# Optimization experiments

Measured on AMD Instinct MI355X. Metric: run time of the kernel, lower is better.

## Reference

```python
import jax, jax.numpy as jnp
import numpy as np

D_MODEL = 1024
N_HEADS = 16
HEAD_DIM = D_MODEL // N_HEADS
SCALE = HEAD_DIM ** -0.5


def setup_inputs() -> dict:
    key = jax.random.key(0)
    ks = jax.random.split(key, 5)
    B, T = 2, 2048
    w_std = D_MODEL ** -0.5  # ~ torch Linear init scale
    return {
        "x": jax.random.normal(ks[0], (B, T, D_MODEL), dtype=jnp.float32),
        "W_q": jax.random.normal(ks[1], (D_MODEL, D_MODEL), dtype=jnp.float32) * w_std,
        "W_k": jax.random.normal(ks[2], (D_MODEL, D_MODEL), dtype=jnp.float32) * w_std,
        "W_v": jax.random.normal(ks[3], (D_MODEL, D_MODEL), dtype=jnp.float32) * w_std,
        "W_o": jax.random.normal(ks[4], (D_MODEL, D_MODEL), dtype=jnp.float32) * w_std,
    }


def reference(x, W_q, W_k, W_v, W_o):
    # torch Linear: y = x @ W.T  (weight stored as (out, in))
    B, T, _ = x.shape

    def split_heads(y):  # (B,T,D) -> (B,H,T,hd)
        return y.reshape(B, T, N_HEADS, HEAD_DIM).transpose(0, 2, 1, 3)

    q = split_heads(x @ W_q.T)
    k = split_heads(x @ W_k.T)
    v = split_heads(x @ W_v.T)

    attn = jnp.einsum("bhqd,bhkd->bhqk", q, k) * SCALE  # (B,H,T,T)
    attn = jax.nn.softmax(attn, axis=-1)
    out = jnp.einsum("bhqk,bhkd->bhqd", attn, v)  # (B,H,T,hd)
    out = out.transpose(0, 2, 1, 3).reshape(B, T, D_MODEL)
    return out @ W_o.T
```

## Files before the change

kernel.cpp:

```cpp
#include <hip/hip_runtime.h>
#include <hip/hip_bf16.h>

#define D_MODEL 1024
#define N_HEADS 16
#define HEAD_DIM 64
#define SEQ 2048
#define BATCH 2

typedef __attribute__((ext_vector_type(8))) short bf16x8;
typedef __attribute__((ext_vector_type(4))) short bf16x4;
typedef __attribute__((ext_vector_type(4))) float f32x4;
typedef __attribute__((ext_vector_type(16))) float f32x16;

typedef __attribute__((address_space(3))) unsigned lds_uint;
typedef __attribute__((address_space(1))) const unsigned global_cuint;

__device__ __forceinline__ void async_cp16(const ushort* g, ushort* l) {
  __builtin_amdgcn_global_load_lds((global_cuint*)g, (lds_uint*)l, 16, 0, 0);
}

__device__ __forceinline__ ushort f2b(float f) {
  union { float f; unsigned u; } x; x.f = f;
  unsigned r = x.u + 0x7fffu + ((x.u >> 16) & 1u);
  return (ushort)(r >> 16);
}

__device__ __forceinline__ unsigned pk2(float a, float b) {
  __hip_bfloat162 h = __float22bfloat162_rn(float2{a, b});
  union { __hip_bfloat162 h; unsigned u; } x; x.h = h;
  return x.u;
}

__device__ __forceinline__ float blo(unsigned u) {
  union { unsigned u; float f; } x; x.u = u << 16; return x.f;
}
__device__ __forceinline__ float bhi(unsigned u) {
  union { unsigned u; float f; } x; x.u = u & 0xffff0000u; return x.f;
}

__device__ __forceinline__ int sigma23(int t) {
  return (t & ~12) | ((t & 4) << 1) | ((t & 8) >> 1);
}

__device__ __forceinline__ int swz64(int row, int colbyte) {
  return row * 64 + ((colbyte ^ ((row & 7) << 4)) >> 1);
}

__global__ __launch_bounds__(256) void cast_all(const float* __restrict__ x,
                                                const float* __restrict__ Wq,
                                                const float* __restrict__ Wk,
                                                const float* __restrict__ Wv,
                                                const float* __restrict__ Wo,
                                                ushort* __restrict__ xb,
                                                ushort* __restrict__ wqkv,
                                                ushort* __restrict__ wob) {
  int idx = blockIdx.x * 256 + threadIdx.x;
  const float* in;
  uint2* out;
  if (idx < (1 << 20)) {
    in = x; out = (uint2*)xb;
  } else {
    int j = idx - (1 << 20);
    int w = j >> 18;
    idx = j & 0x3FFFF;
    switch (w) {
      case 0: in = Wq; out = (uint2*)wqkv; break;
      case 1: in = Wk; out = (uint2*)(wqkv) + (1 << 18); break;
      case 2: in = Wv; out = (uint2*)(wqkv) + (2 << 18); break;
      default: in = Wo; out = (uint2*)wob; break;
    }
  }
  float4 v = ((const float4*)in)[idx];
  uint2 o; o.x = pk2(v.x, v.y); o.y = pk2(v.z, v.w);
  out[idx] = o;
}

__global__ __launch_bounds__(512, 2) void gemm_qkv(const ushort* __restrict__ A,
                                                   const ushort* __restrict__ Bw,
                                                   ushort* __restrict__ Qh,
                                                   ushort* __restrict__ Kh,
                                                   ushort* __restrict__ Vth,
                                                   float qscale) {
  constexpr int K = 1024;
  const int bm = blockIdx.y * 128;
  const int bn = blockIdx.x * 128;
  const int tid = threadIdx.x;
  const int wave = tid >> 6;
  const int lane = tid & 63;
  const int l16 = lane & 15;
  const int quad = lane >> 4;

  __shared__ ushort As[2][128 * 64];
  __shared__ ushort Bs[2][128 * 64];

  const int wm = (wave & 1) * 64;
  const int wn = (wave >> 1) * 32;

  f32x4 acc[4][2];
#pragma unroll
  for (int r = 0; r < 4; ++r)
#pragma unroll
    for (int c = 0; c < 2; ++c) acc[r][c] = (f32x4){0.f, 0.f, 0.f, 0.f};

  const int srow = wave * 8 + (lane >> 3);
  const int csw = (((lane & 7) ^ (lane >> 3)) << 3);

#pragma unroll
  for (int j = 0; j < 2; ++j) {
    async_cp16(A  + (size_t)(bm + j * 64 + srow) * K + csw, &As[0][(j * 64 + wave * 8) * 64]);
    async_cp16(Bw + (size_t)(bn + j * 64 + srow) * K + csw, &Bs[0][(j * 64 + wave * 8) * 64]);
  }

  constexpr int NIT = K / 64;
  for (int kt = 0; kt < NIT; ++kt) {
    __syncthreads();
    const int buf = kt & 1;
    if (kt + 1 < NIT) {
      const int k0 = (kt + 1) * 64;
#pragma unroll
      for (int j = 0; j < 2; ++j) {
        async_cp16(A  + (size_t)(bm + j * 64 + srow) * K + k0 + csw, &As[buf ^ 1][(j * 64 + wave * 8) * 64]);
        async_cp16(Bw + (size_t)(bn + j * 64 + srow) * K + k0 + csw, &Bs[buf ^ 1][(j * 64 + wave * 8) * 64]);
      }
    }

    bf16x8 a[2][4], b[2][2];
#pragma unroll
    for (int ks = 0; ks < 2; ++ks) {
#pragma unroll
      for (int r = 0; r < 4; ++r)
        a[ks][r] = *(const bf16x8*)(&As[buf][swz64(wm + r * 16 + l16, ks * 64 + quad * 16)]);
#pragma unroll
      for (int c = 0; c < 2; ++c)
        b[ks][c] = *(const bf16x8*)(&Bs[buf][swz64(wn + c * 16 + l16, ks * 64 + quad * 16)]);
    }
#pragma unroll
    for (int ks = 0; ks < 2; ++ks)
#pragma unroll
      for (int r = 0; r < 4; ++r)
#pragma unroll
        for (int c = 0; c < 2; ++c)
          acc[r][c] = __builtin_amdgcn_mfma_f32_16x16x32_bf16(a[ks][r], b[ks][c], acc[r][c], 0, 0, 0);
  }

#pragma unroll
  for (int r = 0; r < 4; ++r) {
#pragma unroll
    for (int c = 0; c < 2; ++c) {
      int ncol = bn + wn + c * 16 + l16;
      int w = ncol >> 10;
      int f = ncol & 1023;
      int h = f >> 6, d = f & 63;
      if (w == 2) {
        int m0 = bm + wm + r * 16 + quad * 4;
        int b = m0 >> 11, t0 = m0 & 2047;
        uint2 pp;
        pp.x = pk2(acc[r][c][0], acc[r][c][1]);
        pp.y = pk2(acc[r][c][2], acc[r][c][3]);
        *(uint2*)(&Vth[((size_t)(b * 1024 + f) << 11) + t0]) = pp;
      } else {
#pragma unroll
        for (int rr = 0; rr < 4; ++rr) {
          float v = acc[r][c][rr];
          int m = bm + wm + r * 16 + quad * 4 + rr;
          int b = m >> 11, t = m & 2047;
          if (w == 0)
            Qh[((size_t)(b * 16 + h) * SEQ + t) * 64 + d] = f2b(v * qscale);
          else
            Kh[((size_t)(b * 16 + h) * SEQ + sigma23(t)) * 64 + d] = f2b(v);
        }
      }
    }
  }
}

__global__ __launch_bounds__(256) void gemm_out(const ushort* __restrict__ A,
                                                const ushort* __restrict__ Bw,
                                                float* __restrict__ out) {
  constexpr int K = 1024;
  const int bm = blockIdx.y * 64;
  const int bn = blockIdx.x * 128;
  const int tid = threadIdx.x;
  const int wave = tid >> 6;
  const int lane = tid & 63;
  const int l16 = lane & 15;
  const int quad = lane >> 4;

  __shared__ ushort As[2][64 * 64];
  __shared__ ushort Bs[2][128 * 64];

  const int wm = (wave & 1) * 32;
  const int wn = (wave >> 1) * 64;

  f32x4 acc[2][4];
#pragma unroll
  for (int r = 0; r < 2; ++r)
#pragma unroll
    for (int c = 0; c < 4; ++c) acc[r][c] = (f32x4){0.f, 0.f, 0.f, 0.f};

  const int srow = wave * 8 + (lane >> 3);
  const int csw = (((lane & 7) ^ (lane >> 3)) << 3);

#pragma unroll
  for (int j = 0; j < 2; ++j)
    async_cp16(A + (size_t)(bm + j * 32 + srow) * K + csw, &As[0][(j * 32 + wave * 8) * 64]);
#pragma unroll
  for (int j = 0; j < 4; ++j)
    async_cp16(Bw + (size_t)(bn + j * 32 + srow) * K + csw, &Bs[0][(j * 32 + wave * 8) * 64]);

  constexpr int NIT = K / 64;
  for (int kt = 0; kt < NIT; ++kt) {
    __syncthreads();
    const int buf = kt & 1;
    if (kt + 1 < NIT) {
      const int k0 = (kt + 1) * 64;
#pragma unroll
      for (int j = 0; j < 2; ++j)
        async_cp16(A + (size_t)(bm + j * 32 + srow) * K + k0 + csw, &As[buf ^ 1][(j * 32 + wave * 8) * 64]);
#pragma unroll
      for (int j = 0; j < 4; ++j)
        async_cp16(Bw + (size_t)(bn + j * 32 + srow) * K + k0 + csw, &Bs[buf ^ 1][(j * 32 + wave * 8) * 64]);
    }

    bf16x8 a[2][2], b[2][4];
#pragma unroll
    for (int ks = 0; ks < 2; ++ks) {
#pragma unroll
      for (int r = 0; r < 2; ++r)
        a[ks][r] = *(const bf16x8*)(&As[buf][swz64(wm + r * 16 + l16, ks * 64 + quad * 16)]);
#pragma unroll
      for (int c = 0; c < 4; ++c)
        b[ks][c] = *(const bf16x8*)(&Bs[buf][swz64(wn + c * 16 + l16, ks * 64 + quad * 16)]);
    }
#pragma unroll
    for (int ks = 0; ks < 2; ++ks)
#pragma unroll
      for (int r = 0; r < 2; ++r)
#pragma unroll
        for (int c = 0; c < 4; ++c)
          acc[r][c] = __builtin_amdgcn_mfma_f32_16x16x32_bf16(a[ks][r], b[ks][c], acc[r][c], 0, 0, 0);
  }

#pragma unroll
  for (int r = 0; r < 2; ++r)
#pragma unroll
    for (int c = 0; c < 4; ++c)
#pragma unroll
      for (int rr = 0; rr < 4; ++rr) {
        int m = bm + wm + r * 16 + quad * 4 + rr;
        int n = bn + wn + c * 16 + l16;
        out[(size_t)m * D_MODEL + n] = acc[r][c][rr];
      }
}

__global__ __launch_bounds__(256, 2) void attn_kernel(const ushort* __restrict__ Qh,
                                                      const ushort* __restrict__ Kh,
                                                      const ushort* __restrict__ Vth,
                                                      ushort* __restrict__ O1,
                                                      ushort* __restrict__ O2,
                                                      float* __restrict__ l1,
                                                      float* __restrict__ l2) {
  const int id = blockIdx.x;
  const int stream = id & 63;
  const int qb = id >> 6;
  const int bh = stream >> 1;
  const int half = stream & 1;
  const int q0 = qb * 128;
  ushort* __restrict__ Op = half ? O2 : O1;
  float* __restrict__ lp = half ? l2 : l1;

  const int tid = threadIdx.x;
  const int wave = tid >> 6;
  const int lane = tid & 63;
  const int l31 = lane & 31;
  const int hi = lane >> 5;

  __shared__ ushort KVbuf[2][2][64 * 64];

  bf16x8 qf[4];
#pragma unroll
  for (int dc = 0; dc < 4; ++dc)
    qf[dc] = *(const bf16x8*)(Qh + ((size_t)bh * SEQ + q0 + wave * 32 + l31) * 64 + dc * 16 + hi * 8);

  f32x16 o0 = {0.f, 0.f, 0.f, 0.f, 0.f, 0.f, 0.f, 0.f,
               0.f, 0.f, 0.f, 0.f, 0.f, 0.f, 0.f, 0.f};
  f32x16 o1 = o0;
  float lacc = 0.f;

  const int chunk = wave * 2;
  const int r8 = lane >> 3;
  const int csw = (((lane & 7) ^ r8) << 3);
  const ushort* kbase = Kh + ((size_t)bh * SEQ + half * 1024) * 64;
  const ushort* vbase = Vth + (size_t)bh * 64 * SEQ + half * 1024;
  const ushort* ksrc = kbase + (size_t)(chunk * 8 + r8) * 64 + csw;
  const ushort* vsrc = vbase + (size_t)(chunk * 8 + r8) * SEQ + csw;

  async_cp16(ksrc,           &KVbuf[0][0][chunk * 512]);
  async_cp16(ksrc + 8 * 64,  &KVbuf[0][0][(chunk + 1) * 512]);
  async_cp16(vsrc,           &KVbuf[0][1][chunk * 512]);
  async_cp16(vsrc + 8 * SEQ, &KVbuf[0][1][(chunk + 1) * 512]);

  constexpr int NIT = 1024 / 64;
  for (int kt = 0; kt < NIT; ++kt) {
    __syncthreads();
    const int buf = kt & 1;
    if (kt + 1 < NIT) {
      const ushort* ks = ksrc + (size_t)(kt + 1) * 64 * 64;
      const ushort* vs = vsrc + (kt + 1) * 64;
      async_cp16(ks,           &KVbuf[buf ^ 1][0][chunk * 512]);
      async_cp16(ks + 8 * 64,  &KVbuf[buf ^ 1][0][(chunk + 1) * 512]);
      async_cp16(vs,           &KVbuf[buf ^ 1][1][chunk * 512]);
      async_cp16(vs + 8 * SEQ, &KVbuf[buf ^ 1][1][(chunk + 1) * 512]);
    }
    const ushort* Kt = KVbuf[buf][0];
    const ushort* Vt = KVbuf[buf][1];

#pragma unroll
    for (int kt2 = 0; kt2 < 2; ++kt2) {
      bf16x8 ka0 = *(const bf16x8*)(&Kt[swz64(kt2 * 32 + l31, 0 * 32 + hi * 16)]);
      bf16x8 ka1 = *(const bf16x8*)(&Kt[swz64(kt2 * 32 + l31, 1 * 32 + hi * 16)]);
      bf16x8 ka2 = *(const bf16x8*)(&Kt[swz64(kt2 * 32 + l31, 2 * 32 + hi * 16)]);
      bf16x8 ka3 = *(const bf16x8*)(&Kt[swz64(kt2 * 32 + l31, 3 * 32 + hi * 16)]);
      f32x16 z = {0.f, 0.f, 0.f, 0.f, 0.f, 0.f, 0.f, 0.f,
                  0.f, 0.f, 0.f, 0.f, 0.f, 0.f, 0.f, 0.f};
      z = __builtin_amdgcn_mfma_f32_32x32x16_bf16(ka0, qf[0], z, 0, 0, 0);
      z = __builtin_amdgcn_mfma_f32_32x32x16_bf16(ka1, qf[1], z, 0, 0, 0);
      z = __builtin_amdgcn_mfma_f32_32x32x16_bf16(ka2, qf[2], z, 0, 0, 0);
      z = __builtin_amdgcn_mfma_f32_32x32x16_bf16(ka3, qf[3], z, 0, 0, 0);

      float e[16];
#pragma unroll
      for (int r = 0; r < 16; ++r) e[r] = __builtin_amdgcn_exp2f(z[r]);
      lacc += (((e[0] + e[1]) + (e[2] + e[3])) + ((e[4] + e[5]) + (e[6] + e[7])))
            + (((e[8] + e[9]) + (e[10] + e[11])) + ((e[12] + e[13]) + (e[14] + e[15])));

#pragma unroll
      for (int lw = 0; lw < 2; ++lw) {
        const int base = lw * 8;
        union { unsigned u[4]; bf16x8 v; } pu;
        pu.u[0] = pk2(e[base + 0], e[base + 1]);
        pu.u[1] = pk2(e[base + 2], e[base + 3]);
        pu.u[2] = pk2(e[base + 4], e[base + 5]);
        pu.u[3] = pk2(e[base + 6], e[base + 7]);
        const int wb = (kt2 * 2 + lw) * 32;
        bf16x8 vb0 = *(const bf16x8*)(&Vt[swz64(0 + l31, wb + hi * 16)]);
        bf16x8 vb1 = *(const bf16x8*)(&Vt[swz64(32 + l31, wb + hi * 16)]);
        o0 = __builtin_amdgcn_mfma_f32_32x32x16_bf16(pu.v, vb0, o0, 0, 0, 0);
        o1 = __builtin_amdgcn_mfma_f32_32x32x16_bf16(pu.v, vb1, o1, 0, 0, 0);
      }
    }
  }

  {
    float ltot = lacc + __shfl_xor(lacc, 32, 64);
    if (hi == 0)
      lp[(size_t)bh * SEQ + q0 + wave * 32 + l31] = ltot;
  }

  __syncthreads();
  ushort* Ob = &KVbuf[0][0][0];
#pragma unroll
  for (int r = 0; r < 16; ++r) {
    int row = wave * 32 + (r & 3) + 8 * (r >> 2) + 4 * hi;
    Ob[row * 64 + l31] = f2b(o0[r]);
    Ob[row * 64 + 32 + l31] = f2b(o1[r]);
  }
  __syncthreads();
  {
    uint4* dst = (uint4*)(Op + ((size_t)bh * SEQ + q0) * 64);
    const uint4* src = (const uint4*)Ob;
#pragma unroll
    for (int i = 0; i < 4; ++i)
      dst[i * 256 + tid] = src[i * 256 + tid];
  }
}

__global__ __launch_bounds__(256) void recombine(const ushort* __restrict__ O1,
                                                 const ushort* __restrict__ O2,
                                                 const float* __restrict__ l1,
                                                 const float* __restrict__ l2,
                                                 ushort* __restrict__ ctx) {
  int idx = blockIdx.x * 256 + threadIdx.x;
  int row = idx >> 3;
  int d8 = idx & 7;
  uint4 a = ((const uint4*)O1)[idx];
  uint4 b = ((const uint4*)O2)[idx];
  float linv = 1.f / (l1[row] + l2[row]);
  uint4 res;
  unsigned* ap = (unsigned*)&a;
  unsigned* bp = (unsigned*)&b;
  unsigned* rp = (unsigned*)&res;
#pragma unroll
  for (int i = 0; i < 4; ++i) {
    float lo = (blo(ap[i]) + blo(bp[i])) * linv;
    float hi = (bhi(ap[i]) + bhi(bp[i])) * linv;
    rp[i] = pk2(lo, hi);
  }
  int bh = row >> 11, t = row & 2047;
  int bb = bh >> 4, h = bh & 15;
  ((uint4*)ctx)[(size_t)(bb * SEQ + t) * 128 + h * 8 + d8] = res;
}

extern "C" void kernel_launch(void* const* d_in, const int* in_sizes, int n_in,
                              void* d_out, int out_size, void* d_ws, size_t ws_size,
                              hipStream_t stream) {
  const float* x  = (const float*)d_in[0];
  const float* Wq = (const float*)d_in[1];
  const float* Wk = (const float*)d_in[2];
  const float* Wv = (const float*)d_in[3];
  const float* Wo = (const float*)d_in[4];
  float* out = (float*)d_out;

  char* ws = (char*)d_ws;
  const size_t MB = 1 << 20;
  ushort* xb   = (ushort*)(ws);
  ushort* wqkv = (ushort*)(ws +  8 * MB);
  ushort* wob  = (ushort*)(ws + 14 * MB);
  ushort* Qh   = (ushort*)(ws + 16 * MB);
  ushort* Kh   = (ushort*)(ws + 24 * MB);
  ushort* Vth  = (ushort*)(ws + 32 * MB);
  ushort* ctx  = (ushort*)(ws + 40 * MB);

  ushort* O1 = (ushort*)d_out;
  ushort* O2 = xb;
  float*  l1 = (float*)wqkv;
  float*  l2 = (float*)(ws + 8 * MB + 256 * 1024);

  cast_all<<<8192, 256, 0, stream>>>(x, Wq, Wk, Wv, Wo, xb, wqkv, wob);

  const float qscale = 0.125f * 1.44269504089f;
  gemm_qkv<<<dim3(3072 / 128, 4096 / 128), 512, 0, stream>>>(xb, wqkv, Qh, Kh, Vth, qscale);

  attn_kernel<<<(SEQ / 128) * BATCH * N_HEADS * 2, 256, 0, stream>>>(
      Qh, Kh, Vth, O1, O2, l1, l2);

  recombine<<<(BATCH * N_HEADS * SEQ * 64 / 8) / 256, 256, 0, stream>>>(O1, O2, l1, l2, ctx);

  gemm_out<<<dim3(1024 / 128, 4096 / 64), 256, 0, stream>>>(ctx, wob, out);
}
```

Measured before the change: 185.6 us.

## Process two 32-row query groups per wave in attention, halving block threads

The attention kernel now runs 2 waves (128 threads) per block instead of 4, and each wave handles 64 query rows as two 32-row groups. The K and V fragments loaded from shared memory are reused across both groups, which cuts LDS reads per MFMA. Each thread now issues twice as many async copies for the K/V tile. The cost is higher register pressure from doubled Q fragments and accumulators, and fewer waves per block to hide latency.

```diff
diff --git a/kernel.cpp b/kernel.cpp
--- a/kernel.cpp
+++ b/kernel.cpp
@@ -253,7 +253,7 @@
       }
 }
 
-__global__ __launch_bounds__(256, 2) void attn_kernel(const ushort* __restrict__ Qh,
+__global__ __launch_bounds__(128, 2) void attn_kernel(const ushort* __restrict__ Qh,
                                                       const ushort* __restrict__ Kh,
                                                       const ushort* __restrict__ Vth,
                                                       ushort* __restrict__ O1,
@@ -277,28 +277,35 @@
 
   __shared__ ushort KVbuf[2][2][64 * 64];
 
-  bf16x8 qf[4];
-#pragma unroll
-  for (int dc = 0; dc < 4; ++dc)
-    qf[dc] = *(const bf16x8*)(Qh + ((size_t)bh * SEQ + q0 + wave * 32 + l31) * 64 + dc * 16 + hi * 8);
-
-  f32x16 o0 = {0.f, 0.f, 0.f, 0.f, 0.f, 0.f, 0.f, 0.f,
-               0.f, 0.f, 0.f, 0.f, 0.f, 0.f, 0.f, 0.f};
-  f32x16 o1 = o0;
-  float lacc = 0.f;
-
-  const int chunk = wave * 2;
+  bf16x8 qf[2][4];
+#pragma unroll
+  for (int g = 0; g < 2; ++g)
+#pragma unroll
+    for (int dc = 0; dc < 4; ++dc)
+      qf[g][dc] = *(const bf16x8*)(Qh + ((size_t)bh * SEQ + q0 + wave * 64 + g * 32 + l31) * 64 + dc * 16 + hi * 8);
+
+  f32x16 o[2][2];
+#pragma unroll
+  for (int g = 0; g < 2; ++g)
+#pragma unroll
+    for (int dh = 0; dh < 2; ++dh)
+      o[g][dh] = (f32x16){0.f, 0.f, 0.f, 0.f, 0.f, 0.f, 0.f, 0.f,
+                          0.f, 0.f, 0.f, 0.f, 0.f, 0.f, 0.f, 0.f};
+  float lacc[2] = {0.f, 0.f};
+
+  const int cb = wave * 4;
   const int r8 = lane >> 3;
   const int csw = (((lane & 7) ^ r8) << 3);
   const ushort* kbase = Kh + ((size_t)bh * SEQ + half * 1024) * 64;
   const ushort* vbase = Vth + (size_t)bh * 64 * SEQ + half * 1024;
-  const ushort* ksrc = kbase + (size_t)(chunk * 8 + r8) * 64 + csw;
-  const ushort* vsrc = vbase + (size_t)(chunk * 8 + r8) * SEQ + csw;
-
-  async_cp16(ksrc,           &KVbuf[0][0][chunk * 512]);
-  async_cp16(ksrc + 8 * 64,  &KVbuf[0][0][(chunk + 1) * 512]);
-  async_cp16(vsrc,           &KVbuf[0][1][chunk * 512]);
-  async_cp16(vsrc + 8 * SEQ, &KVbuf[0][1][(chunk + 1) * 512]);
+  const ushort* ksrc = kbase + (size_t)(cb * 8 + r8) * 64 + csw;
+  const ushort* vsrc = vbase + (size_t)(cb * 8 + r8) * SEQ + csw;
+
+#pragma unroll
+  for (int jk = 0; jk < 4; ++jk) {
+    async_cp16(ksrc + (size_t)jk * 8 * 64,  &KVbuf[0][0][(cb + jk) * 512]);
+    async_cp16(vsrc + (size_t)jk * 8 * SEQ, &KVbuf[0][1][(cb + jk) * 512]);
+  }
 
   constexpr int NIT = 1024 / 64;
   for (int kt = 0; kt < NIT; ++kt) {
@@ -307,10 +314,11 @@
     if (kt + 1 < NIT) {
       const ushort* ks = ksrc + (size_t)(kt + 1) * 64 * 64;
       const ushort* vs = vsrc + (kt + 1) * 64;
-      async_cp16(ks,           &KVbuf[buf ^ 1][0][chunk * 512]);
-      async_cp16(ks + 8 * 64,  &KVbuf[buf ^ 1][0][(chunk + 1) * 512]);
-      async_cp16(vs,           &KVbuf[buf ^ 1][1][chunk * 512]);
-      async_cp16(vs + 8 * SEQ, &KVbuf[buf ^ 1][1][(chunk + 1) * 512]);
+#pragma unroll
+      for (int jk = 0; jk < 4; ++jk) {
+        async_cp16(ks + (size_t)jk * 8 * 64,  &KVbuf[buf ^ 1][0][(cb + jk) * 512]);
+        async_cp16(vs + (size_t)jk * 8 * SEQ, &KVbuf[buf ^ 1][1][(cb + jk) * 512]);
+      }
     }
     const ushort* Kt = KVbuf[buf][0];
     const ushort* Vt = KVbuf[buf][1];
@@ -321,57 +329,68 @@
       bf16x8 ka1 = *(const bf16x8*)(&Kt[swz64(kt2 * 32 + l31, 1 * 32 + hi * 16)]);
       bf16x8 ka2 = *(const bf16x8*)(&Kt[swz64(kt2 * 32 + l31, 2 * 32 + hi * 16)]);
       bf16x8 ka3 = *(const bf16x8*)(&Kt[swz64(kt2 * 32 + l31, 3 * 32 + hi * 16)]);
-      f32x16 z = {0.f, 0.f, 0.f, 0.f, 0.f, 0.f, 0.f, 0.f,
-                  0.f, 0.f, 0.f, 0.f, 0.f, 0.f, 0.f, 0.f};
-      z = __builtin_amdgcn_mfma_f32_32x32x16_bf16(ka0, qf[0], z, 0, 0, 0);
-      z = __builtin_amdgcn_mfma_f32_32x32x16_bf16(ka1, qf[1], z, 0, 0, 0);
-      z = __builtin_amdgcn_mfma_f32_32x32x16_bf16(ka2, qf[2], z, 0, 0, 0);
-      z = __builtin_amdgcn_mfma_f32_32x32x16_bf16(ka3, qf[3], z, 0, 0, 0);
-
-      float e[16];
-#pragma unroll
-      for (int r = 0; r < 16; ++r) e[r] = __builtin_amdgcn_exp2f(z[r]);
-      lacc += (((e[0] + e[1]) + (e[2] + e[3])) + ((e[4] + e[5]) + (e[6] + e[7])))
-            + (((e[8] + e[9]) + (e[10] + e[11])) + ((e[12] + e[13]) + (e[14] + e[15])));
-
+      bf16x8 vb[2][2];
 #pragma unroll
       for (int lw = 0; lw < 2; ++lw) {
-        const int base = lw * 8;
-        union { unsigned u[4]; bf16x8 v; } pu;
-        pu.u[0] = pk2(e[base + 0], e[base + 1]);
-        pu.u[1] = pk2(e[base + 2], e[base + 3]);
-        pu.u[2] = pk2(e[base + 4], e[base + 5]);
-        pu.u[3] = pk2(e[base + 6], e[base + 7]);
         const int wb = (kt2 * 2 + lw) * 32;
-        bf16x8 vb0 = *(const bf16x8*)(&Vt[swz64(0 + l31, wb + hi * 16)]);
-        bf16x8 vb1 = *(const bf16x8*)(&Vt[swz64(32 + l31, wb + hi * 16)]);
-        o0 = __builtin_amdgcn_mfma_f32_32x32x16_bf16(pu.v, vb0, o0, 0, 0, 0);
-        o1 = __builtin_amdgcn_mfma_f32_32x32x16_bf16(pu.v, vb1, o1, 0, 0, 0);
-      }
-    }
-  }
-
-  {
-    float ltot = lacc + __shfl_xor(lacc, 32, 64);
+        vb[lw][0] = *(const bf16x8*)(&Vt[swz64(0 + l31, wb + hi * 16)]);
+        vb[lw][1] = *(const bf16x8*)(&Vt[swz64(32 + l31, wb + hi * 16)]);
+      }
+
+#pragma unroll
+      for (int g = 0; g < 2; ++g) {
+        f32x16 z = {0.f, 0.f, 0.f, 0.f, 0.f, 0.f, 0.f, 0.f,
+                    0.f, 0.f, 0.f, 0.f, 0.f, 0.f, 0.f, 0.f};
+        z = __builtin_amdgcn_mfma_f32_32x32x16_bf16(ka0, qf[g][0], z, 0, 0, 0);
+        z = __builtin_amdgcn_mfma_f32_32x32x16_bf16(ka1, qf[g][1], z, 0, 0, 0);
+        z = __builtin_amdgcn_mfma_f32_32x32x16_bf16(ka2, qf[g][2], z, 0, 0, 0);
+        z = __builtin_amdgcn_mfma_f32_32x32x16_bf16(ka3, qf[g][3], z, 0, 0, 0);
+
+        float e[16];
+#pragma unroll
+        for (int r = 0; r < 16; ++r) e[r] = __builtin_amdgcn_exp2f(z[r]);
+        lacc[g] += (((e[0] + e[1]) + (e[2] + e[3])) + ((e[4] + e[5]) + (e[6] + e[7])))
+                 + (((e[8] + e[9]) + (e[10] + e[11])) + ((e[12] + e[13]) + (e[14] + e[15])));
+
+#pragma unroll
+        for (int lw = 0; lw < 2; ++lw) {
+          const int base = lw * 8;
+          union { unsigned u[4]; bf16x8 v; } pu;
+          pu.u[0] = pk2(e[base + 0], e[base + 1]);
+          pu.u[1] = pk2(e[base + 2], e[base + 3]);
+          pu.u[2] = pk2(e[base + 4], e[base + 5]);
+          pu.u[3] = pk2(e[base + 6], e[base + 7]);
+          o[g][0] = __builtin_amdgcn_mfma_f32_32x32x16_bf16(pu.v, vb[lw][0], o[g][0], 0, 0, 0);
+          o[g][1] = __builtin_amdgcn_mfma_f32_32x32x16_bf16(pu.v, vb[lw][1], o[g][1], 0, 0, 0);
+        }
+      }
+    }
+  }
+
+#pragma unroll
+  for (int g = 0; g < 2; ++g) {
+    float ltot = lacc[g] + __shfl_xor(lacc[g], 32, 64);
     if (hi == 0)
-      lp[(size_t)bh * SEQ + q0 + wave * 32 + l31] = ltot;
+      lp[(size_t)bh * SEQ + q0 + wave * 64 + g * 32 + l31] = ltot;
   }
 
   __syncthreads();
   ushort* Ob = &KVbuf[0][0][0];
 #pragma unroll
-  for (int r = 0; r < 16; ++r) {
-    int row = wave * 32 + (r & 3) + 8 * (r >> 2) + 4 * hi;
-    Ob[row * 64 + l31] = f2b(o0[r]);
-    Ob[row * 64 + 32 + l31] = f2b(o1[r]);
-  }
+  for (int g = 0; g < 2; ++g)
+#pragma unroll
+    for (int r = 0; r < 16; ++r) {
+      int row = wave * 64 + g * 32 + (r & 3) + 8 * (r >> 2) + 4 * hi;
+      Ob[row * 64 + l31] = f2b(o[g][0][r]);
+      Ob[row * 64 + 32 + l31] = f2b(o[g][1][r]);
+    }
   __syncthreads();
   {
     uint4* dst = (uint4*)(Op + ((size_t)bh * SEQ + q0) * 64);
     const uint4* src = (const uint4*)Ob;
 #pragma unroll
-    for (int i = 0; i < 4; ++i)
-      dst[i * 256 + tid] = src[i * 256 + tid];
+    for (int i = 0; i < 8; ++i)
+      dst[i * 128 + tid] = src[i * 128 + tid];
   }
 }
 
@@ -431,7 +450,7 @@
   const float qscale = 0.125f * 1.44269504089f;
   gemm_qkv<<<dim3(3072 / 128, 4096 / 128), 512, 0, stream>>>(xb, wqkv, Qh, Kh, Vth, qscale);
 
-  attn_kernel<<<(SEQ / 128) * BATCH * N_HEADS * 2, 256, 0, stream>>>(
+  attn_kernel<<<(SEQ / 128) * BATCH * N_HEADS * 2, 128, 0, stream>>>(
       Qh, Kh, Vth, O1, O2, l1, l2);
 
   recombine<<<(BATCH * N_HEADS * SEQ * 64 / 8) / 256, 256, 0, stream>>>(O1, O2, l1, l2, ctx);
```

New measurement: 186.7 us. No clear change (+0.6%).

## Fuse split-attention recombine into output projection GEMM A-tile loading

Applied to the files above, without the earlier changes.

Removes the separate recombine kernel and instead has gemm_out load the two partial attention outputs and softmax denominators, combine and normalize them in registers, and write the bf16 A tile to LDS. The A operand loads are software-pipelined two stages ahead via register staging rather than async global-to-LDS copies. This removes a kernel launch and the ctx round trip through memory. In exchange, each gemm_out block (8 column blocks share the same rows) redoes the recombine arithmetic and reads twice as much A data, and the A path becomes synchronous register loads.

```diff
diff --git a/kernel.cpp b/kernel.cpp
--- a/kernel.cpp
+++ b/kernel.cpp
@@ -174,7 +174,10 @@
   }
 }
 
-__global__ __launch_bounds__(256) void gemm_out(const ushort* __restrict__ A,
+__global__ __launch_bounds__(256) void gemm_out(const ushort* __restrict__ O1,
+                                                const ushort* __restrict__ O2,
+                                                const float* __restrict__ l1,
+                                                const float* __restrict__ l2,
                                                 const ushort* __restrict__ Bw,
                                                 float* __restrict__ out) {
   constexpr int K = 1024;
@@ -199,28 +202,69 @@
     for (int c = 0; c < 4; ++c) acc[r][c] = (f32x4){0.f, 0.f, 0.f, 0.f};
 
   const int srow = wave * 8 + (lane >> 3);
-  const int csw = (((lane & 7) ^ (lane >> 3)) << 3);
-
-#pragma unroll
-  for (int j = 0; j < 2; ++j)
-    async_cp16(A + (size_t)(bm + j * 32 + srow) * K + csw, &As[0][(j * 32 + wave * 8) * 64]);
+  const int slot = lane & 7;
+  const int csw = ((slot ^ (lane >> 3)) << 3);
+
+  uint4 a1[2], a2[2];
+  float lv[2];
+
+  size_t rb[2];
+  {
+#pragma unroll
+    for (int j = 0; j < 2; ++j) {
+      int m = bm + j * 32 + srow;
+      int b = m >> 11, t = m & 2047;
+      rb[j] = (size_t)(b * 16) * SEQ + t;
+    }
+  }
+
+#define LOAD_A(h)                                                         \
+  {                                                                       \
+    _Pragma("unroll")                                                     \
+    for (int j = 0; j < 2; ++j) {                                         \
+      size_t rowbase = rb[j] + (size_t)(h) * SEQ;                         \
+      a1[j] = *(const uint4*)(O1 + rowbase * 64 + slot * 8);              \
+      a2[j] = *(const uint4*)(O2 + rowbase * 64 + slot * 8);              \
+      lv[j] = l1[rowbase] + l2[rowbase];                                  \
+    }                                                                     \
+  }
+
+#define WRITE_A(bufi)                                                     \
+  {                                                                       \
+    _Pragma("unroll")                                                     \
+    for (int j = 0; j < 2; ++j) {                                         \
+      float linv = 1.f / lv[j];                                           \
+      uint4 res;                                                          \
+      unsigned* ap = (unsigned*)&a1[j];                                   \
+      unsigned* bp = (unsigned*)&a2[j];                                   \
+      unsigned* rp = (unsigned*)&res;                                     \
+      _Pragma("unroll")                                                   \
+      for (int i = 0; i < 4; ++i)                                         \
+        rp[i] = pk2((blo(ap[i]) + blo(bp[i])) * linv,                     \
+                    (bhi(ap[i]) + bhi(bp[i])) * linv);                    \
+      *(uint4*)(&As[bufi][swz64(j * 32 + srow, slot * 16)]) = res;        \
+    }                                                                     \
+  }
+
+  LOAD_A(0);
+  WRITE_A(0);
 #pragma unroll
   for (int j = 0; j < 4; ++j)
     async_cp16(Bw + (size_t)(bn + j * 32 + srow) * K + csw, &Bs[0][(j * 32 + wave * 8) * 64]);
+  LOAD_A(1);
 
   constexpr int NIT = K / 64;
   for (int kt = 0; kt < NIT; ++kt) {
     __syncthreads();
     const int buf = kt & 1;
     if (kt + 1 < NIT) {
+      WRITE_A(buf ^ 1);
       const int k0 = (kt + 1) * 64;
-#pragma unroll
-      for (int j = 0; j < 2; ++j)
-        async_cp16(A + (size_t)(bm + j * 32 + srow) * K + k0 + csw, &As[buf ^ 1][(j * 32 + wave * 8) * 64]);
 #pragma unroll
       for (int j = 0; j < 4; ++j)
         async_cp16(Bw + (size_t)(bn + j * 32 + srow) * K + k0 + csw, &Bs[buf ^ 1][(j * 32 + wave * 8) * 64]);
     }
+    if (kt + 2 < NIT) LOAD_A(kt + 2);
 
     bf16x8 a[2][2], b[2][4];
 #pragma unroll
@@ -251,6 +295,8 @@
         int n = bn + wn + c * 16 + l16;
         out[(size_t)m * D_MODEL + n] = acc[r][c][rr];
       }
+#undef LOAD_A
+#undef WRITE_A
 }
 
 __global__ __launch_bounds__(256, 2) void attn_kernel(const ushort* __restrict__ Qh,
@@ -375,32 +421,6 @@
   }
 }
 
-__global__ __launch_bounds__(256) void recombine(const ushort* __restrict__ O1,
-                                                 const ushort* __restrict__ O2,
-                                                 const float* __restrict__ l1,
-                                                 const float* __restrict__ l2,
-                                                 ushort* __restrict__ ctx) {
-  int idx = blockIdx.x * 256 + threadIdx.x;
-  int row = idx >> 3;
-  int d8 = idx & 7;
-  uint4 a = ((const uint4*)O1)[idx];
-  uint4 b = ((const uint4*)O2)[idx];
-  float linv = 1.f / (l1[row] + l2[row]);
-  uint4 res;
-  unsigned* ap = (unsigned*)&a;
-  unsigned* bp = (unsigned*)&b;
-  unsigned* rp = (unsigned*)&res;
-#pragma unroll
-  for (int i = 0; i < 4; ++i) {
-    float lo = (blo(ap[i]) + blo(bp[i])) * linv;
-    float hi = (bhi(ap[i]) + bhi(bp[i])) * linv;
-    rp[i] = pk2(lo, hi);
-  }
-  int bh = row >> 11, t = row & 2047;
-  int bb = bh >> 4, h = bh & 15;
-  ((uint4*)ctx)[(size_t)(bb * SEQ + t) * 128 + h * 8 + d8] = res;
-}
-
 extern "C" void kernel_launch(void* const* d_in, const int* in_sizes, int n_in,
                               void* d_out, int out_size, void* d_ws, size_t ws_size,
                               hipStream_t stream) {
@@ -419,9 +439,8 @@
   ushort* Qh   = (ushort*)(ws + 16 * MB);
   ushort* Kh   = (ushort*)(ws + 24 * MB);
   ushort* Vth  = (ushort*)(ws + 32 * MB);
-  ushort* ctx  = (ushort*)(ws + 40 * MB);
-
-  ushort* O1 = (ushort*)d_out;
+
+  ushort* O1 = (ushort*)(ws + 40 * MB);
   ushort* O2 = xb;
   float*  l1 = (float*)wqkv;
   float*  l2 = (float*)(ws + 8 * MB + 256 * 1024);
@@ -434,7 +453,5 @@
   attn_kernel<<<(SEQ / 128) * BATCH * N_HEADS * 2, 256, 0, stream>>>(
       Qh, Kh, Vth, O1, O2, l1, l2);
 
-  recombine<<<(BATCH * N_HEADS * SEQ * 64 / 8) / 256, 256, 0, stream>>>(O1, O2, l1, l2, ctx);
-
-  gemm_out<<<dim3(1024 / 128, 4096 / 64), 256, 0, stream>>>(ctx, wob, out);
-}
+  gemm_out<<<dim3(1024 / 128, 4096 / 64), 256, 0, stream>>>(O1, O2, l1, l2, wob, out);
+}
```

Result: slower. 194.5 us (+4.8%).

## Drop split-KV attention and recombine kernel; normalize and write ctx in-kernel

Applied to the files above, without the earlier changes.

The attention kernel no longer splits the key range into two halves with separate partial outputs. Each block now walks the full 2048-key sequence, normalizes by the row sum kept in shared memory, and writes directly into the head-interleaved ctx layout. This removes the recombine launch and the round trip of partial outputs and sums through global memory. In exchange the grid halves to 512 blocks with twice as many iterations each, which lowers parallelism on a GPU with many compute units.

```diff
diff --git a/kernel.cpp b/kernel.cpp
--- a/kernel.cpp
+++ b/kernel.cpp
@@ -256,18 +256,12 @@
 __global__ __launch_bounds__(256, 2) void attn_kernel(const ushort* __restrict__ Qh,
                                                       const ushort* __restrict__ Kh,
                                                       const ushort* __restrict__ Vth,
-                                                      ushort* __restrict__ O1,
-                                                      ushort* __restrict__ O2,
-                                                      float* __restrict__ l1,
-                                                      float* __restrict__ l2) {
+                                                      ushort* __restrict__ ctx) {
   const int id = blockIdx.x;
-  const int stream = id & 63;
-  const int qb = id >> 6;
-  const int bh = stream >> 1;
-  const int half = stream & 1;
+  const int bh = id & 31;
+  const int qb = id >> 5;
   const int q0 = qb * 128;
-  ushort* __restrict__ Op = half ? O2 : O1;
-  float* __restrict__ lp = half ? l2 : l1;
+  const int b = bh >> 4, h = bh & 15;
 
   const int tid = threadIdx.x;
   const int wave = tid >> 6;
@@ -276,6 +270,7 @@
   const int hi = lane >> 5;
 
   __shared__ ushort KVbuf[2][2][64 * 64];
+  __shared__ float Ls[128];
 
   bf16x8 qf[4];
 #pragma unroll
@@ -290,8 +285,8 @@
   const int chunk = wave * 2;
   const int r8 = lane >> 3;
   const int csw = (((lane & 7) ^ r8) << 3);
-  const ushort* kbase = Kh + ((size_t)bh * SEQ + half * 1024) * 64;
-  const ushort* vbase = Vth + (size_t)bh * 64 * SEQ + half * 1024;
+  const ushort* kbase = Kh + (size_t)bh * SEQ * 64;
+  const ushort* vbase = Vth + (size_t)bh * 64 * SEQ;
   const ushort* ksrc = kbase + (size_t)(chunk * 8 + r8) * 64 + csw;
   const ushort* vsrc = vbase + (size_t)(chunk * 8 + r8) * SEQ + csw;
 
@@ -300,7 +295,7 @@
   async_cp16(vsrc,           &KVbuf[0][1][chunk * 512]);
   async_cp16(vsrc + 8 * SEQ, &KVbuf[0][1][(chunk + 1) * 512]);
 
-  constexpr int NIT = 1024 / 64;
+  constexpr int NIT = SEQ / 64;
   for (int kt = 0; kt < NIT; ++kt) {
     __syncthreads();
     const int buf = kt & 1;
@@ -354,7 +349,7 @@
   {
     float ltot = lacc + __shfl_xor(lacc, 32, 64);
     if (hi == 0)
-      lp[(size_t)bh * SEQ + q0 + wave * 32 + l31] = ltot;
+      Ls[wave * 32 + l31] = ltot;
   }
 
   __syncthreads();
@@ -362,43 +357,21 @@
 #pragma unroll
   for (int r = 0; r < 16; ++r) {
     int row = wave * 32 + (r & 3) + 8 * (r >> 2) + 4 * hi;
-    Ob[row * 64 + l31] = f2b(o0[r]);
-    Ob[row * 64 + 32 + l31] = f2b(o1[r]);
+    float linv = 1.f / Ls[row];
+    Ob[row * 64 + l31] = f2b(o0[r] * linv);
+    Ob[row * 64 + 32 + l31] = f2b(o1[r] * linv);
   }
   __syncthreads();
   {
-    uint4* dst = (uint4*)(Op + ((size_t)bh * SEQ + q0) * 64);
+    uint4* dst = (uint4*)ctx;
     const uint4* src = (const uint4*)Ob;
 #pragma unroll
-    for (int i = 0; i < 4; ++i)
-      dst[i * 256 + tid] = src[i * 256 + tid];
-  }
-}
-
-__global__ __launch_bounds__(256) void recombine(const ushort* __restrict__ O1,
-                                                 const ushort* __restrict__ O2,
-                                                 const float* __restrict__ l1,
-                                                 const float* __restrict__ l2,
-                                                 ushort* __restrict__ ctx) {
-  int idx = blockIdx.x * 256 + threadIdx.x;
-  int row = idx >> 3;
-  int d8 = idx & 7;
-  uint4 a = ((const uint4*)O1)[idx];
-  uint4 b = ((const uint4*)O2)[idx];
-  float linv = 1.f / (l1[row] + l2[row]);
-  uint4 res;
-  unsigned* ap = (unsigned*)&a;
-  unsigned* bp = (unsigned*)&b;
-  unsigned* rp = (unsigned*)&res;
-#pragma unroll
-  for (int i = 0; i < 4; ++i) {
-    float lo = (blo(ap[i]) + blo(bp[i])) * linv;
-    float hi = (bhi(ap[i]) + bhi(bp[i])) * linv;
-    rp[i] = pk2(lo, hi);
-  }
-  int bh = row >> 11, t = row & 2047;
-  int bb = bh >> 4, h = bh & 15;
-  ((uint4*)ctx)[(size_t)(bb * SEQ + t) * 128 + h * 8 + d8] = res;
+    for (int i = 0; i < 4; ++i) {
+      int idx = i * 256 + tid;
+      int row = idx >> 3, d8 = idx & 7;
+      dst[(size_t)(b * SEQ + q0 + row) * 128 + h * 8 + d8] = src[idx];
+    }
+  }
 }
 
 extern "C" void kernel_launch(void* const* d_in, const int* in_sizes, int n_in,
@@ -421,20 +394,12 @@
   ushort* Vth  = (ushort*)(ws + 32 * MB);
   ushort* ctx  = (ushort*)(ws + 40 * MB);
 
-  ushort* O1 = (ushort*)d_out;
-  ushort* O2 = xb;
-  float*  l1 = (float*)wqkv;
-  float*  l2 = (float*)(ws + 8 * MB + 256 * 1024);
-
   cast_all<<<8192, 256, 0, stream>>>(x, Wq, Wk, Wv, Wo, xb, wqkv, wob);
 
   const float qscale = 0.125f * 1.44269504089f;
   gemm_qkv<<<dim3(3072 / 128, 4096 / 128), 512, 0, stream>>>(xb, wqkv, Qh, Kh, Vth, qscale);
 
-  attn_kernel<<<(SEQ / 128) * BATCH * N_HEADS * 2, 256, 0, stream>>>(
-      Qh, Kh, Vth, O1, O2, l1, l2);
-
-  recombine<<<(BATCH * N_HEADS * SEQ * 64 / 8) / 256, 256, 0, stream>>>(O1, O2, l1, l2, ctx);
+  attn_kernel<<<(SEQ / 128) * BATCH * N_HEADS, 256, 0, stream>>>(Qh, Kh, Vth, ctx);
 
   gemm_out<<<dim3(1024 / 128, 4096 / 64), 256, 0, stream>>>(ctx, wob, out);
 }
```

Measured after the change: 182.7 us. Within noise of the previous version (-1.6%).
